# Optimization experiments

Measured on AMD Instinct MI355X. Metric: run time of the kernel, lower is better.

The kernel has to match this reference:

```python
import jax, jax.numpy as jnp
import numpy as np

SEQ, D = 4096, 1024  # vector_size == dimension == 1024


def setup_inputs() -> dict:
    key = jax.random.key(0)
    ks = jax.random.split(key, 7)
    s = 1.0 / np.sqrt(D)
    return {
        "X": jax.random.normal(ks[0], (SEQ, D), dtype=jnp.float32),
        "Wq": jax.random.normal(ks[1], (D, D), dtype=jnp.float32) * s,
        "bq": jax.random.normal(ks[2], (D,), dtype=jnp.float32) * s,
        "Wk": jax.random.normal(ks[3], (D, D), dtype=jnp.float32) * s,
        "bk": jax.random.normal(ks[4], (D,), dtype=jnp.float32) * s,
        "Wv": jax.random.normal(ks[5], (D, D), dtype=jnp.float32) * s,
        "bv": jax.random.normal(ks[6], (D,), dtype=jnp.float32) * s,
    }


def reference(X, Wq, bq, Wk, bk, Wv, bv):
    # Batched QKV projections (nn.Linear: x @ W^T + b), replacing the per-vector loop.
    Q = X @ Wq.T + bq            # [S, D]
    K = X @ Wk.T + bk            # [S, D]
    V = X @ Wv.T + bv            # [S, D]
    scale = 1.0 / jnp.sqrt(jnp.asarray(D, dtype=X.dtype))
    scores = (Q @ K.T) * scale   # [S, S]
    attn = jax.nn.softmax(scores, axis=1)
    return attn @ V              # [S, D]
```

## Files before the change

kernel.cpp:

```cpp
#include <hip/hip_runtime.h>
#include <hip/hip_bf16.h>
#include <stdint.h>


typedef __bf16 bf16_t;
typedef __bf16 bf16x4 __attribute__((ext_vector_type(4)));
typedef __bf16 bf16x8 __attribute__((ext_vector_type(8)));
typedef float f32x4 __attribute__((ext_vector_type(4)));

#define AS1 __attribute__((address_space(1)))
#define AS3 __attribute__((address_space(3)))

__device__ __forceinline__ void async_ld16(const void* g, void* l) {
  __builtin_amdgcn_global_load_lds((AS1 void*)g, (AS3 void*)l, 16, 0, 0);
}

#define BAR() __builtin_amdgcn_s_barrier()
#define LGKM0() asm volatile("s_waitcnt lgkmcnt(0)" ::: "memory")

template <int MODE>
__global__ __launch_bounds__(512, 2) void gemm8(
    const bf16_t* __restrict__ A, const bf16_t* __restrict__ B, const int ld,
    const int Klen, bf16_t* __restrict__ o0, bf16_t* __restrict__ o1,
    bf16_t* __restrict__ o2, const float* __restrict__ b0,
    const float* __restrict__ b1, const float* __restrict__ b2,
    float* __restrict__ fout, float* __restrict__ rowsum) {
  extern __shared__ bf16_t smem[];

  const int t = threadIdx.x;
  const int lane = t & 63;
  const int wave = t >> 6;
  const int wm = wave >> 2;
  const int wn = wave & 3;
  const int q = lane >> 4;
  const int l16 = lane & 15;
  const int xf = l16 & 7;

  int m0, n0, k0 = 0, zz = 0;
  const int bid = blockIdx.x;
  if constexpr (MODE == 0) {
    const int x = bid & 7, sl = bid >> 3;
    m0 = ((x >> 1) * 4 + (sl & 3)) * 256;
    n0 = ((x & 1) * 6 + (sl >> 2)) * 256;
  } else if constexpr (MODE == 1) {
    const int x = bid & 7, sl = bid >> 3;
    m0 = ((x >> 2) * 8 + (sl >> 2)) * 256;
    n0 = ((x & 3) * 4 + (sl & 3)) * 256;
  } else {
    const int x = bid & 7, sl = bid >> 3;
    zz = x >> 1;
    m0 = ((x & 1) * 8 + (sl >> 2)) * 256;
    n0 = (sl & 3) * 256;
    k0 = zz * Klen;
  }

  const int srow = t >> 3;
  const int c8s = ((t & 7) ^ (srow & 7)) * 8;
  const bf16_t* Ab = A + (size_t)(m0 + srow) * ld + k0 + c8s;
  const bf16_t* Bb = B + (size_t)(n0 + srow) * ld + k0 + c8s;
  const int tl8 = t * 8;

  const int aoff = (wm * 128 + l16) * 64;
  const int boff = (wn * 64 + l16) * 64;
  const int c0 = (q ^ xf) * 8;
  const int c1 = ((4 + q) ^ xf) * 8;

  f32x4 acc[8][4];
  const f32x4 zero4 = {0.f, 0.f, 0.f, 0.f};
#pragma unroll
  for (int i = 0; i < 8; ++i)
#pragma unroll
    for (int j = 0; j < 4; ++j) acc[i][j] = zero4;

  const int NT = Klen >> 6;
  bf16_t* buf0 = smem;
  bf16_t* buf1 = smem + 32768;

  async_ld16(Ab, buf0 + tl8);
  async_ld16(Ab + (size_t)64 * ld, buf0 + 4096 + tl8);
  async_ld16(Ab + (size_t)128 * ld, buf0 + 8192 + tl8);
  async_ld16(Ab + (size_t)192 * ld, buf0 + 12288 + tl8);
  async_ld16(Bb, buf0 + 16384 + tl8);
  async_ld16(Bb + (size_t)64 * ld, buf0 + 16384 + 4096 + tl8);
  async_ld16(Bb + (size_t)128 * ld, buf0 + 16384 + 8192 + tl8);
  async_ld16(Bb + (size_t)192 * ld, buf0 + 16384 + 12288 + tl8);
  async_ld16(Ab + 64, buf1 + tl8);
  async_ld16(Ab + (size_t)128 * ld + 64, buf1 + 8192 + tl8);
  async_ld16(Bb + 64, buf1 + 16384 + tl8);
  async_ld16(Bb + (size_t)64 * ld + 64, buf1 + 16384 + 4096 + tl8);
  async_ld16(Bb + (size_t)128 * ld + 64, buf1 + 16384 + 8192 + tl8);
  async_ld16(Bb + (size_t)192 * ld + 64, buf1 + 16384 + 12288 + tl8);
  asm volatile("s_waitcnt vmcnt(6)" ::: "memory");
  BAR();

  for (int T = 0; T < NT; ++T) {
    bf16_t* Ac = (T & 1) ? buf1 : buf0;
    bf16_t* An = (T & 1) ? buf0 : buf1;
    bf16_t* Bc = Ac + 16384;
    const int k1 = (T + 1) << 6;
    const int k2 = (T + 2) << 6;
    const bool s1 = (T + 1) < NT;
    const bool s2 = (T + 2) < NT;

    bf16x8 ra0[4], ra1[4], rc0[4], rc1[4], rb0[4], rb1[4];

#pragma unroll
    for (int im = 0; im < 4; ++im)
      ra0[im] = *(const bf16x8*)(Ac + aoff + im * 1024 + c0);
#pragma unroll
    for (int j = 0; j < 4; ++j)
      rb0[j] = *(const bf16x8*)(Bc + boff + j * 1024 + c0);
    if (s1) {
      async_ld16(Ab + (size_t)64 * ld + k1, An + 4096 + tl8);
      async_ld16(Ab + (size_t)192 * ld + k1, An + 12288 + tl8);
    }
    BAR();
    LGKM0();
    __builtin_amdgcn_s_setprio(1);
#pragma unroll
    for (int im = 0; im < 4; ++im)
#pragma unroll
      for (int j = 0; j < 4; ++j)
        acc[im][j] = __builtin_amdgcn_mfma_f32_16x16x32_bf16(
            ra0[im], rb0[j], acc[im][j], 0, 0, 0);
    __builtin_amdgcn_s_setprio(0);
    BAR();

#pragma unroll
    for (int im = 0; im < 4; ++im)
      ra1[im] = *(const bf16x8*)(Ac + aoff + im * 1024 + c1);
#pragma unroll
    for (int j = 0; j < 4; ++j)
      rb1[j] = *(const bf16x8*)(Bc + boff + j * 1024 + c1);
    BAR();
    LGKM0();
    __builtin_amdgcn_s_setprio(1);
#pragma unroll
    for (int im = 0; im < 4; ++im)
#pragma unroll
      for (int j = 0; j < 4; ++j)
        acc[im][j] = __builtin_amdgcn_mfma_f32_16x16x32_bf16(
            ra1[im], rb1[j], acc[im][j], 0, 0, 0);
    __builtin_amdgcn_s_setprio(0);
    BAR();

#pragma unroll
    for (int im = 0; im < 4; ++im)
      rc0[im] = *(const bf16x8*)(Ac + aoff + (im + 4) * 1024 + c0);
    if (s2) {
      async_ld16(Ab + k2, Ac + tl8);
      async_ld16(Ab + (size_t)128 * ld + k2, Ac + 8192 + tl8);
      async_ld16(Bb + k2, Bc + tl8);
      async_ld16(Bb + (size_t)64 * ld + k2, Bc + 4096 + tl8);
    }
    BAR();
    LGKM0();
    __builtin_amdgcn_s_setprio(1);
#pragma unroll
    for (int im = 0; im < 4; ++im)
#pragma unroll
      for (int j = 0; j < 4; ++j)
        acc[4 + im][j] = __builtin_amdgcn_mfma_f32_16x16x32_bf16(
            rc0[im], rb0[j], acc[4 + im][j], 0, 0, 0);
    __builtin_amdgcn_s_setprio(0);
    BAR();

#pragma unroll
    for (int im = 0; im < 4; ++im)
      rc1[im] = *(const bf16x8*)(Ac + aoff + (im + 4) * 1024 + c1);
    if (s2) {
      async_ld16(Bb + (size_t)128 * ld + k2, Bc + 8192 + tl8);
      async_ld16(Bb + (size_t)192 * ld + k2, Bc + 12288 + tl8);
    }
    BAR();
    LGKM0();
    __builtin_amdgcn_s_setprio(1);
#pragma unroll
    for (int im = 0; im < 4; ++im)
#pragma unroll
      for (int j = 0; j < 4; ++j)
        acc[4 + im][j] = __builtin_amdgcn_mfma_f32_16x16x32_bf16(
            rc1[im], rb1[j], acc[4 + im][j], 0, 0, 0);
    __builtin_amdgcn_s_setprio(0);
    if (s2) {
      asm volatile("s_waitcnt vmcnt(6)" ::: "memory");
    } else {
      asm volatile("s_waitcnt vmcnt(0)" ::: "memory");
    }
    BAR();
  }

  const int mW = m0 + wm * 128 + q * 4;

  if constexpr (MODE == 0) {
    const int sel = n0 >> 10;
    const int nl0 = (n0 & 1023) + wn * 64 + l16;
    if (sel < 2) {
      const float* bias = (sel == 0) ? b0 : b1;
      const float sc = (sel == 0) ? 0.03125f : 1.0f;
      bf16_t* dst = (sel == 0) ? o0 : o1;
      float bb[4];
#pragma unroll
      for (int j = 0; j < 4; ++j) bb[j] = bias[nl0 + j * 16];
#pragma unroll
      for (int im = 0; im < 8; ++im) {
        const int mr = mW + im * 16;
#pragma unroll
        for (int r = 0; r < 4; ++r)
#pragma unroll
          for (int j = 0; j < 4; ++j)
            dst[(size_t)(mr + r) * 1024 + nl0 + j * 16] =
                (bf16_t)((acc[im][j][r] + bb[j]) * sc);
      }
    } else {
      bf16_t* vs = smem;
      const int dg0 = n0 & 1023;
#pragma unroll
      for (int h = 0; h < 2; ++h) {
        if ((wn >> 1) == h) {
#pragma unroll
          for (int j = 0; j < 4; ++j) {
            const int dl = (wn & 1) * 64 + j * 16 + l16;
            const float bb = b2[dg0 + h * 128 + dl];
#pragma unroll
            for (int im = 0; im < 8; ++im) {
              bf16x4 v;
#pragma unroll
              for (int r = 0; r < 4; ++r) v[r] = (bf16_t)(acc[im][j][r] + bb);
              *(bf16x4*)(vs + dl * 264 + wm * 128 + im * 16 + q * 4) = v;
            }
          }
        }
        __syncthreads();
#pragma unroll
        for (int rr = 0; rr < 8; ++rr) {
          const int task = rr * 512 + t;
          const int row = task >> 5, ck = task & 31;
          *(bf16x8*)(o2 + (size_t)(dg0 + h * 128 + row) * 4096 + m0 + ck * 8) =
              *(const bf16x8*)(vs + row * 264 + ck * 8);
        }
        __syncthreads();
      }
    }
  } else if constexpr (MODE == 1) {
    float ps[8][4];
#pragma unroll
    for (int im = 0; im < 8; ++im)
#pragma unroll
      for (int r = 0; r < 4; ++r) ps[im][r] = 0.f;
    const int nb = n0 + wn * 64 + l16;
#pragma unroll
    for (int im = 0; im < 8; ++im) {
      const int mr = mW + im * 16;
#pragma unroll
      for (int r = 0; r < 4; ++r)
#pragma unroll
        for (int j = 0; j < 4; ++j) {
          const float e = __expf(acc[im][j][r]);
          ps[im][r] += e;
          o0[(size_t)(mr + r) * 4096 + nb + j * 16] = (bf16_t)e;
        }
    }
#pragma unroll
    for (int im = 0; im < 8; ++im)
#pragma unroll
      for (int r = 0; r < 4; ++r) {
        float v = ps[im][r];
        v += __shfl_xor(v, 1);
        v += __shfl_xor(v, 2);
        v += __shfl_xor(v, 4);
        v += __shfl_xor(v, 8);
        ps[im][r] = v;
      }
    if (l16 == 0) {
#pragma unroll
      for (int im = 0; im < 8; ++im)
#pragma unroll
        for (int r = 0; r < 4; ++r)
          atomicAdd(rowsum + mW + im * 16 + r, ps[im][r]);
    }
  } else {
    float inv[8][4];
#pragma unroll
    for (int im = 0; im < 8; ++im)
#pragma unroll
      for (int r = 0; r < 4; ++r)
        inv[im][r] = 1.0f / rowsum[mW + im * 16 + r];
    const int nb = n0 + wn * 64 + l16;
    if (zz < 3) {
      bf16_t* pp = (zz == 0) ? o0 : ((zz == 1) ? o1 : o2);
#pragma unroll
      for (int im = 0; im < 8; ++im) {
        const int mr = mW + im * 16;
#pragma unroll
        for (int r = 0; r < 4; ++r) {
          const float iv = inv[im][r];
#pragma unroll
          for (int j = 0; j < 4; ++j)
            pp[(size_t)(mr + r) * 1024 + nb + j * 16] =
                (bf16_t)(acc[im][j][r] * iv);
        }
      }
    } else {
#pragma unroll
      for (int im = 0; im < 8; ++im) {
        const int mr = mW + im * 16;
#pragma unroll
        for (int r = 0; r < 4; ++r) {
          const float iv = inv[im][r];
#pragma unroll
          for (int j = 0; j < 4; ++j)
            fout[(size_t)(mr + r) * 1024 + nb + j * 16] = acc[im][j][r] * iv;
        }
      }
    }
  }
}

__global__ __launch_bounds__(256) void cvt_all(
    const float* __restrict__ X, const float* __restrict__ Wq,
    const float* __restrict__ Wk, const float* __restrict__ Wv,
    bf16_t* __restrict__ Xb, bf16_t* __restrict__ Wb,
    float* __restrict__ rowsum) {
  int i = blockIdx.x * 256 + threadIdx.x;
  if (i >= 1835008) {
    rowsum[i - 1835008] = 0.f;
    return;
  }
  const float* src;
  bf16_t* dst;
  int off;
  if (i < 1048576) {
    src = X; dst = Xb; off = i;
  } else {
    const int w = i - 1048576;
    const int sel = w >> 18;
    off = w & 0x3FFFF;
    src = (sel == 0) ? Wq : ((sel == 1) ? Wk : Wv);
    dst = Wb + (size_t)sel * (1024 * 1024);
  }
  const float4 v = ((const float4*)src)[off];
  bf16x4 o;
  o[0] = (bf16_t)v.x; o[1] = (bf16_t)v.y; o[2] = (bf16_t)v.z; o[3] = (bf16_t)v.w;
  ((bf16x4*)dst)[off] = o;
}

__global__ __launch_bounds__(256) void reduce_out(
    const bf16_t* __restrict__ p0, const bf16_t* __restrict__ p1,
    const bf16_t* __restrict__ p2, float* __restrict__ out) {
  const int i = blockIdx.x * 256 + threadIdx.x;
  const bf16x8 a = ((const bf16x8*)p0)[i];
  const bf16x8 b = ((const bf16x8*)p1)[i];
  const bf16x8 c = ((const bf16x8*)p2)[i];
  float4 lo = ((const float4*)out)[2 * i];
  float4 hi = ((const float4*)out)[2 * i + 1];
  lo.x += (float)a[0] + (float)b[0] + (float)c[0];
  lo.y += (float)a[1] + (float)b[1] + (float)c[1];
  lo.z += (float)a[2] + (float)b[2] + (float)c[2];
  lo.w += (float)a[3] + (float)b[3] + (float)c[3];
  hi.x += (float)a[4] + (float)b[4] + (float)c[4];
  hi.y += (float)a[5] + (float)b[5] + (float)c[5];
  hi.z += (float)a[6] + (float)b[6] + (float)c[6];
  hi.w += (float)a[7] + (float)b[7] + (float)c[7];
  ((float4*)out)[2 * i] = lo;
  ((float4*)out)[2 * i + 1] = hi;
}

extern "C" void kernel_launch(void* const* d_in, const int* in_sizes, int n_in,
                              void* d_out, int out_size, void* d_ws,
                              size_t ws_size, hipStream_t stream) {
  const int S = 4096, D = 1024;
  const float* X  = (const float*)d_in[0];
  const float* Wq = (const float*)d_in[1];
  const float* bq = (const float*)d_in[2];
  const float* Wk = (const float*)d_in[3];
  const float* bk = (const float*)d_in[4];
  const float* Wv = (const float*)d_in[5];
  const float* bv = (const float*)d_in[6];
  float* out = (float*)d_out;

  bf16_t* Xb = (bf16_t*)d_ws;
  bf16_t* Wb = Xb + (size_t)S * D;
  bf16_t* Qb = Wb + (size_t)3 * D * D;
  bf16_t* Kb = Qb + (size_t)S * D;
  bf16_t* Vt = Kb + (size_t)S * D;
  bf16_t* Sc = Vt + (size_t)D * S;
  float* rowsum = (float*)(Sc + (size_t)S * S);

  static int attr_set = 0;
  if (!attr_set) {
    attr_set = 1;
    (void)hipFuncSetAttribute(reinterpret_cast<const void*>(gemm8<0>),
                              hipFuncAttributeMaxDynamicSharedMemorySize,
                              131072);
    (void)hipFuncSetAttribute(reinterpret_cast<const void*>(gemm8<1>),
                              hipFuncAttributeMaxDynamicSharedMemorySize,
                              131072);
    (void)hipFuncSetAttribute(reinterpret_cast<const void*>(gemm8<2>),
                              hipFuncAttributeMaxDynamicSharedMemorySize,
                              131072);
  }

  cvt_all<<<7184, 256, 0, stream>>>(X, Wq, Wk, Wv, Xb, Wb, rowsum);

  gemm8<0><<<192, 512, 131072, stream>>>(
      Xb, Wb, D, D, Qb, Kb, Vt, bq, bk, bv, nullptr, nullptr);
  gemm8<1><<<256, 512, 131072, stream>>>(
      Qb, Kb, D, D, Sc, nullptr, nullptr, nullptr, nullptr, nullptr, nullptr,
      rowsum);
  gemm8<2><<<256, 512, 131072, stream>>>(
      Sc, Vt, S, S / 4, Xb, Qb, Kb, nullptr, nullptr, nullptr, out, rowsum);
  reduce_out<<<S * D / 8 / 256, 256, 0, stream>>>(Xb, Qb, Kb, out);
}
```

Measured before the change: 215.7 us.

## Replace hand-scheduled interleaved GEMM main loop with simple double-buffered loop

Drops the two-tiles-ahead prefetch. That schedule split each 64-wide K tile into four barrier-separated MFMA phases, with async LDS loads slotted between phases and explicit vmcnt/lgkmcnt waits plus s_setprio. The new loop uses a single next-tile prefetch, loads all A and B fragments per K half, runs 32 MFMAs, and ends with one __syncthreads per tile. It reduces barrier count and code complexity. The cost is less overlap between global loads, LDS reads and MFMA issue, since the end-of-tile sync likely drains the prefetch. It also raises register pressure from holding 8 A fragments at once.

```diff
diff --git a/kernel.cpp b/kernel.cpp
--- a/kernel.cpp
+++ b/kernel.cpp
@@ -14,9 +14,6 @@
 __device__ __forceinline__ void async_ld16(const void* g, void* l) {
   __builtin_amdgcn_global_load_lds((AS1 void*)g, (AS3 void*)l, 16, 0, 0);
 }
-
-#define BAR() __builtin_amdgcn_s_barrier()
-#define LGKM0() asm volatile("s_waitcnt lgkmcnt(0)" ::: "memory")
 
 template <int MODE>
 __global__ __launch_bounds__(512, 2) void gemm8(
@@ -76,118 +73,44 @@
   bf16_t* buf0 = smem;
   bf16_t* buf1 = smem + 32768;
 
-  async_ld16(Ab, buf0 + tl8);
-  async_ld16(Ab + (size_t)64 * ld, buf0 + 4096 + tl8);
-  async_ld16(Ab + (size_t)128 * ld, buf0 + 8192 + tl8);
-  async_ld16(Ab + (size_t)192 * ld, buf0 + 12288 + tl8);
-  async_ld16(Bb, buf0 + 16384 + tl8);
-  async_ld16(Bb + (size_t)64 * ld, buf0 + 16384 + 4096 + tl8);
-  async_ld16(Bb + (size_t)128 * ld, buf0 + 16384 + 8192 + tl8);
-  async_ld16(Bb + (size_t)192 * ld, buf0 + 16384 + 12288 + tl8);
-  async_ld16(Ab + 64, buf1 + tl8);
-  async_ld16(Ab + (size_t)128 * ld + 64, buf1 + 8192 + tl8);
-  async_ld16(Bb + 64, buf1 + 16384 + tl8);
-  async_ld16(Bb + (size_t)64 * ld + 64, buf1 + 16384 + 4096 + tl8);
-  async_ld16(Bb + (size_t)128 * ld + 64, buf1 + 16384 + 8192 + tl8);
-  async_ld16(Bb + (size_t)192 * ld + 64, buf1 + 16384 + 12288 + tl8);
-  asm volatile("s_waitcnt vmcnt(6)" ::: "memory");
-  BAR();
+  auto STAGE = [&](int T, bf16_t* buf) {
+    const size_t kk = (size_t)(T << 6);
+    async_ld16(Ab + kk, buf + tl8);
+    async_ld16(Ab + (size_t)64 * ld + kk, buf + 4096 + tl8);
+    async_ld16(Ab + (size_t)128 * ld + kk, buf + 8192 + tl8);
+    async_ld16(Ab + (size_t)192 * ld + kk, buf + 12288 + tl8);
+    async_ld16(Bb + kk, buf + 16384 + tl8);
+    async_ld16(Bb + (size_t)64 * ld + kk, buf + 16384 + 4096 + tl8);
+    async_ld16(Bb + (size_t)128 * ld + kk, buf + 16384 + 8192 + tl8);
+    async_ld16(Bb + (size_t)192 * ld + kk, buf + 16384 + 12288 + tl8);
+  };
+
+  STAGE(0, buf0);
+  __syncthreads();
 
   for (int T = 0; T < NT; ++T) {
-    bf16_t* Ac = (T & 1) ? buf1 : buf0;
-    bf16_t* An = (T & 1) ? buf0 : buf1;
-    bf16_t* Bc = Ac + 16384;
-    const int k1 = (T + 1) << 6;
-    const int k2 = (T + 2) << 6;
-    const bool s1 = (T + 1) < NT;
-    const bool s2 = (T + 2) < NT;
-
-    bf16x8 ra0[4], ra1[4], rc0[4], rc1[4], rb0[4], rb1[4];
-
-#pragma unroll
-    for (int im = 0; im < 4; ++im)
-      ra0[im] = *(const bf16x8*)(Ac + aoff + im * 1024 + c0);
-#pragma unroll
-    for (int j = 0; j < 4; ++j)
-      rb0[j] = *(const bf16x8*)(Bc + boff + j * 1024 + c0);
-    if (s1) {
-      async_ld16(Ab + (size_t)64 * ld + k1, An + 4096 + tl8);
-      async_ld16(Ab + (size_t)192 * ld + k1, An + 12288 + tl8);
-    }
-    BAR();
-    LGKM0();
-    __builtin_amdgcn_s_setprio(1);
-#pragma unroll
-    for (int im = 0; im < 4; ++im)
+    bf16_t* cur = (T & 1) ? buf1 : buf0;
+    bf16_t* nxt = (T & 1) ? buf0 : buf1;
+    if (T + 1 < NT) STAGE(T + 1, nxt);
+
+#pragma unroll
+    for (int s = 0; s < 2; ++s) {
+      const int cs = (s == 0) ? c0 : c1;
+      bf16x8 fa[8], fb[4];
+#pragma unroll
+      for (int im = 0; im < 8; ++im)
+        fa[im] = *(const bf16x8*)(cur + aoff + im * 1024 + cs);
 #pragma unroll
       for (int j = 0; j < 4; ++j)
-        acc[im][j] = __builtin_amdgcn_mfma_f32_16x16x32_bf16(
-            ra0[im], rb0[j], acc[im][j], 0, 0, 0);
-    __builtin_amdgcn_s_setprio(0);
-    BAR();
-
-#pragma unroll
-    for (int im = 0; im < 4; ++im)
-      ra1[im] = *(const bf16x8*)(Ac + aoff + im * 1024 + c1);
-#pragma unroll
-    for (int j = 0; j < 4; ++j)
-      rb1[j] = *(const bf16x8*)(Bc + boff + j * 1024 + c1);
-    BAR();
-    LGKM0();
-    __builtin_amdgcn_s_setprio(1);
-#pragma unroll
-    for (int im = 0; im < 4; ++im)
-#pragma unroll
-      for (int j = 0; j < 4; ++j)
-        acc[im][j] = __builtin_amdgcn_mfma_f32_16x16x32_bf16(
-            ra1[im], rb1[j], acc[im][j], 0, 0, 0);
-    __builtin_amdgcn_s_setprio(0);
-    BAR();
-
-#pragma unroll
-    for (int im = 0; im < 4; ++im)
-      rc0[im] = *(const bf16x8*)(Ac + aoff + (im + 4) * 1024 + c0);
-    if (s2) {
-      async_ld16(Ab + k2, Ac + tl8);
-      async_ld16(Ab + (size_t)128 * ld + k2, Ac + 8192 + tl8);
-      async_ld16(Bb + k2, Bc + tl8);
-      async_ld16(Bb + (size_t)64 * ld + k2, Bc + 4096 + tl8);
-    }
-    BAR();
-    LGKM0();
-    __builtin_amdgcn_s_setprio(1);
-#pragma unroll
-    for (int im = 0; im < 4; ++im)
-#pragma unroll
-      for (int j = 0; j < 4; ++j)
-        acc[4 + im][j] = __builtin_amdgcn_mfma_f32_16x16x32_bf16(
-            rc0[im], rb0[j], acc[4 + im][j], 0, 0, 0);
-    __builtin_amdgcn_s_setprio(0);
-    BAR();
-
-#pragma unroll
-    for (int im = 0; im < 4; ++im)
-      rc1[im] = *(const bf16x8*)(Ac + aoff + (im + 4) * 1024 + c1);
-    if (s2) {
-      async_ld16(Bb + (size_t)128 * ld + k2, Bc + 8192 + tl8);
-      async_ld16(Bb + (size_t)192 * ld + k2, Bc + 12288 + tl8);
-    }
-    BAR();
-    LGKM0();
-    __builtin_amdgcn_s_setprio(1);
-#pragma unroll
-    for (int im = 0; im < 4; ++im)
-#pragma unroll
-      for (int j = 0; j < 4; ++j)
-        acc[4 + im][j] = __builtin_amdgcn_mfma_f32_16x16x32_bf16(
-            rc1[im], rb1[j], acc[4 + im][j], 0, 0, 0);
-    __builtin_amdgcn_s_setprio(0);
-    if (s2) {
-      asm volatile("s_waitcnt vmcnt(6)" ::: "memory");
-    } else {
-      asm volatile("s_waitcnt vmcnt(0)" ::: "memory");
-    }
-    BAR();
+        fb[j] = *(const bf16x8*)(cur + 16384 + boff + j * 1024 + cs);
+#pragma unroll
+      for (int im = 0; im < 8; ++im)
+#pragma unroll
+        for (int j = 0; j < 4; ++j)
+          acc[im][j] = __builtin_amdgcn_mfma_f32_16x16x32_bf16(
+              fa[im], fb[j], acc[im][j], 0, 0, 0);
+    }
+    __syncthreads();
   }
 
   const int mW = m0 + wm * 128 + q * 4;
```

New measurement: 205.0 us. 1.05x faster.
